# Kernel optimization log

Measured on AMD Instinct MI355X. Metric: run time of the kernel, lower is better.

Reference implementation:

```python
import jax, jax.numpy as jnp
import numpy as np

J = 24
ROOT = 0
# SMPL kinematic tree parents
PARENTS = [-1, 0, 0, 0, 1, 2, 3, 4, 5, 6, 7, 8, 9, 9, 9, 12, 13, 14, 16, 17, 18, 19, 20, 21]
RES_SCALE = 0.1


def rodrigues(rvec):
    """Axis-angle (..., 3) -> rotation matrix (..., 3, 3)."""
    theta = jnp.linalg.norm(rvec, axis=-1, keepdims=True)          # (...,1)
    axis = rvec / jnp.maximum(theta, 1e-8)
    x, y, z = axis[..., 0], axis[..., 1], axis[..., 2]
    zero = jnp.zeros_like(x)
    K = jnp.stack([zero, -z, y, z, zero, -x, -y, x, zero], axis=-1)
    K = K.reshape(rvec.shape[:-1] + (3, 3))
    s = jnp.sin(theta)[..., None]
    c = jnp.cos(theta)[..., None]
    I = jnp.eye(3, dtype=rvec.dtype)
    return I + s * K + (1.0 - c) * (K @ K)


def _make_T(R, t):
    """(B,3,3),(B,3) -> (B,4,4) homogeneous transform."""
    B = R.shape[0]
    top = jnp.concatenate([R, t[..., None]], axis=-1)              # (B,3,4)
    bottom = jnp.broadcast_to(jnp.array([0., 0., 0., 1.], R.dtype), (B, 1, 4))
    return jnp.concatenate([top, bottom], axis=-2)


def calculate_kinematic(rest_pose, rvecs, root_locs):
    """rest_pose (J,3), rvecs (B,J,3), root_locs (B,3) -> kp (B,J,3), skts (B,J,4,4).
    Sequential tree-structured chain, unrolled over the 24 joints."""
    R = rodrigues(rvecs)                                           # (B,J,3,3)
    B = rvecs.shape[0]
    l2w = [None] * J
    l2w[ROOT] = _make_T(R[:, ROOT], root_locs)
    for j in range(1, J):
        p = PARENTS[j]
        t_local = jnp.broadcast_to(rest_pose[j] - rest_pose[p], (B, 3))
        l2w[j] = l2w[p] @ _make_T(R[:, j], t_local)
    l2w = jnp.stack(l2w, axis=1)                                   # (B,J,4,4)
    kp = l2w[..., :3, 3]                                           # (B,J,3)
    # skts = inverse(l2w) = [R^T, -R^T t]
    Rt = jnp.swapaxes(l2w[..., :3, :3], -1, -2)
    t_inv = -(Rt @ kp[..., None])                                  # (B,J,3,1)
    top = jnp.concatenate([Rt, t_inv], axis=-1)                    # (B,J,3,4)
    bottom = jnp.broadcast_to(jnp.array([0., 0., 0., 1.], l2w.dtype), (B, J, 1, 4))
    skts = jnp.concatenate([top, bottom], axis=-2)                 # (B,J,4,4)
    return kp, skts


def setup_inputs() -> dict:
    key = jax.random.key(0)
    ks = jax.random.split(key, 12)
    N, NU, E, W = 131072, 16384, 16, 128
    skip = N // NU
    din, dout = J * 3 + E, J * 3 + 3
    bones = jax.random.normal(ks[0], (N, J, 3), jnp.float32) * 0.2
    pelvis_buf = jax.random.normal(ks[1], (NU, 3), jnp.float32)
    kp_idxs = jnp.arange(N, dtype=jnp.int64) // skip
    rest_pose = jax.random.normal(ks[2], (J, 3), jnp.float32) * 0.3
    rest_pose = rest_pose.at[ROOT].set(0.0)
    # kp3d root must match pelvis buffer (original asserts allclose)
    kp3d = jnp.zeros((N, J, 3), jnp.float32).at[:, ROOT].set(pelvis_buf[kp_idxs])
    emb_table = jax.random.normal(ks[3], (NU, E), jnp.float32) * 0.02
    def lin(k, fan_in, fan_out):
        lim = 1.0 / np.sqrt(fan_in)
        k1, k2 = jax.random.split(k)
        return (jax.random.uniform(k1, (fan_in, fan_out), jnp.float32, -lim, lim),
                jax.random.uniform(k2, (fan_out,), jnp.float32, -lim, lim))
    W0, b0 = lin(ks[4], din, W)
    W1, b1 = lin(ks[5], W, W)
    W2, b2 = lin(ks[6], W, W)
    W3, b3 = lin(ks[7], W, dout)
    return dict(bones=bones, kp3d=kp3d, kp_idxs=kp_idxs, emb_table=emb_table,
                pelvis_buf=pelvis_buf, rest_pose=rest_pose,
                W0=W0, b0=b0, W1=W1, b1=b1, W2=W2, b2=b2, W3=W3, b3=b3,
                N_unique=NU)


def reference(bones, kp3d, kp_idxs, emb_table, pelvis_buf, rest_pose,
              W0, b0, W1, b1, W2, b2, W3, b3, N_unique):
    N = bones.shape[0]
    skip = N // N_unique
    rvecs = bones[::skip].reshape(N_unique, J * 3)                 # (Nu, 72)
    kp_u = kp_idxs[::skip]
    embs = emb_table[kp_u]                                         # (Nu, 16)
    pelvis = pelvis_buf[kp_u]                                      # (Nu, 3)
    x = jnp.concatenate([rvecs, embs], axis=-1)
    h = jax.nn.relu(x @ W0 + b0)
    h = jax.nn.relu(h @ W1 + b1)
    h = jax.nn.relu(h @ W2 + b2)
    residual = (h @ W3 + b3) * RES_SCALE                           # (Nu, 75)
    rvecs = (rvecs + residual[:, :J * 3]).reshape(N_unique, J, 3)
    pelvis = pelvis + residual[:, J * 3:]
    kp, skts = calculate_kinematic(rest_pose, rvecs, pelvis)
    # expand unique poses back to full batch ('i s ... -> (i s) ...')
    kp = jnp.repeat(kp, skip, axis=0)                              # (N,J,3)
    skts = jnp.repeat(skts, skip, axis=0)                          # (N,J,4,4)
    rvecs = jnp.repeat(rvecs, skip, axis=0)                        # (N,J,3)
    return kp, skts, rvecs
```

## Files before the change

kernel.cpp:

```cpp
#include <hip/hip_runtime.h>
#include <hip/hip_bf16.h>

typedef unsigned short u16;
using f32x4 = __attribute__((ext_vector_type(4))) float;
using s16x8 = __attribute__((ext_vector_type(8))) short;
using u32x4 = __attribute__((ext_vector_type(4))) unsigned int;

#define JNT 24
#define STRX 104
#define STRH 136

__device__ __forceinline__ u16 f2bf(float f) {
    unsigned int x; __builtin_memcpy(&x, &f, 4);
    unsigned int lsb = (x >> 16) & 1u;
    x += 0x7fffu + lsb;
    return (u16)(x >> 16);
}

__global__ void prep_weights(const float* __restrict__ W0, const float* __restrict__ W1,
                             const float* __restrict__ W2, const float* __restrict__ W3,
                             u16* __restrict__ wst) {
    int i = blockIdx.x * 256 + threadIdx.x;
    if (i < 12288) { int n = i / 96, k = i - n * 96; wst[i] = (k < 88) ? f2bf(W0[k * 128 + n]) : (u16)0; return; }
    i -= 12288;
    if (i < 16384) { int n = i >> 7, k = i & 127; wst[12288 + i] = f2bf(W1[k * 128 + n]); return; }
    i -= 16384;
    if (i < 16384) { int n = i >> 7, k = i & 127; wst[28672 + i] = f2bf(W2[k * 128 + n]); return; }
    i -= 16384;
    if (i < 10240) { int n = i >> 7, k = i & 127; wst[45056 + i] = (n < 75) ? f2bf(W3[k * 75 + n]) : (u16)0; }
}

template<int BASE, int CNT>
__device__ __forceinline__ void mlp_l3(const u16* __restrict__ H, const u16* __restrict__ W3t,
                                       const float* __restrict__ b3, float* __restrict__ res_s,
                                       int lr, int lk, int drow) {
    f32x4 acc[CNT];
#pragma unroll
    for (int t = 0; t < CNT; ++t) {
        int col = (BASE + t) * 16 + lr;
        float bv = (col < 75) ? b3[col] : 0.f;
        acc[t] = (f32x4){bv, bv, bv, bv};
    }
#pragma unroll
    for (int ks = 0; ks < 4; ++ks) {
        s16x8 a = *(const s16x8*)&H[lr * STRH + ks * 32 + lk];
#pragma unroll
        for (int t = 0; t < CNT; ++t) {
            s16x8 b = *(const s16x8*)&W3t[((BASE + t) * 16 + lr) * 128 + ks * 32 + lk];
            acc[t] = __builtin_amdgcn_mfma_f32_16x16x32_bf16(a, b, acc[t], 0, 0, 0);
        }
    }
#pragma unroll
    for (int t = 0; t < CNT; ++t) {
        int col = (BASE + t) * 16 + lr;
        if (col < 75) {
#pragma unroll
            for (int q = 0; q < 4; ++q)
                res_s[(drow + q) * 80 + col] = acc[t][q] * 0.1f;
        }
    }
}

__device__ const int KPARP[32] = {0,0,0,0,1,2,3,4,5,6,7,8,9,9,9,12,13,14,16,17,18,19,20,21,0,0,0,0,0,0,0,0};
__device__ const int KDEPP[32] = {0,1,1,1,2,2,2,3,3,3,4,4,4,4,4,5,5,5,6,6,7,7,8,8,99,99,99,99,99,99,99,99};

__global__ __launch_bounds__(256, 3)
void fused_kernel(const float* __restrict__ bones, const float* __restrict__ emb,
                  const float* __restrict__ pelvis, const float* __restrict__ rest,
                  const float* __restrict__ b0, const float* __restrict__ b1,
                  const float* __restrict__ b2, const float* __restrict__ b3,
                  const u16* __restrict__ wst, float* __restrict__ out,
                  int N, int bstride) {
    __shared__ __align__(16) unsigned char smem[22016];
    float* res_s = (float*)smem;
    u16* Xs = (u16*)(smem + 5120);
    u16* H1 = (u16*)(smem + 8448);
    u16* H2 = (u16*)(smem + 12800);
    float* so8 = (float*)(smem + 5120);

    const int tid = threadIdx.x;
    const int row0 = blockIdx.x * 16;

    for (int i = tid; i < 16 * 96; i += 256) {
        int r = i / 96, c = i - r * 96;
        int u = row0 + r;
        float v = 0.f;
        if (c < 72)      v = bones[(size_t)u * bstride + c];
        else if (c < 88) v = emb[(size_t)u * 16 + (c - 72)];
        Xs[r * STRX + c] = f2bf(v);
    }
    __syncthreads();

    const int lane = tid & 63;
    const int wave = tid >> 6;
    const int lr = lane & 15;
    const int lk = (lane >> 4) * 8;
    const int drow = (lane >> 4) * 4;
    const u16* W0t = wst;
    const u16* W1t = wst + 12288;
    const u16* W2t = wst + 28672;
    const u16* W3t = wst + 45056;

    {
        f32x4 acc[2];
#pragma unroll
        for (int t = 0; t < 2; ++t) { float bv = b0[(wave * 2 + t) * 16 + lr]; acc[t] = (f32x4){bv, bv, bv, bv}; }
#pragma unroll
        for (int ks = 0; ks < 3; ++ks) {
            s16x8 a = *(const s16x8*)&Xs[lr * STRX + ks * 32 + lk];
#pragma unroll
            for (int t = 0; t < 2; ++t) {
                s16x8 b = *(const s16x8*)&W0t[((wave * 2 + t) * 16 + lr) * 96 + ks * 32 + lk];
                acc[t] = __builtin_amdgcn_mfma_f32_16x16x32_bf16(a, b, acc[t], 0, 0, 0);
            }
        }
#pragma unroll
        for (int t = 0; t < 2; ++t)
#pragma unroll
            for (int q = 0; q < 4; ++q)
                H1[(drow + q) * STRH + (wave * 2 + t) * 16 + lr] = f2bf(fmaxf(acc[t][q], 0.f));
    }
    __syncthreads();
    {
        f32x4 acc[2];
#pragma unroll
        for (int t = 0; t < 2; ++t) { float bv = b1[(wave * 2 + t) * 16 + lr]; acc[t] = (f32x4){bv, bv, bv, bv}; }
#pragma unroll
        for (int ks = 0; ks < 4; ++ks) {
            s16x8 a = *(const s16x8*)&H1[lr * STRH + ks * 32 + lk];
#pragma unroll
            for (int t = 0; t < 2; ++t) {
                s16x8 b = *(const s16x8*)&W1t[((wave * 2 + t) * 16 + lr) * 128 + ks * 32 + lk];
                acc[t] = __builtin_amdgcn_mfma_f32_16x16x32_bf16(a, b, acc[t], 0, 0, 0);
            }
        }
#pragma unroll
        for (int t = 0; t < 2; ++t)
#pragma unroll
            for (int q = 0; q < 4; ++q)
                H2[(drow + q) * STRH + (wave * 2 + t) * 16 + lr] = f2bf(fmaxf(acc[t][q], 0.f));
    }
    __syncthreads();
    {
        f32x4 acc[2];
#pragma unroll
        for (int t = 0; t < 2; ++t) { float bv = b2[(wave * 2 + t) * 16 + lr]; acc[t] = (f32x4){bv, bv, bv, bv}; }
#pragma unroll
        for (int ks = 0; ks < 4; ++ks) {
            s16x8 a = *(const s16x8*)&H2[lr * STRH + ks * 32 + lk];
#pragma unroll
            for (int t = 0; t < 2; ++t) {
                s16x8 b = *(const s16x8*)&W2t[((wave * 2 + t) * 16 + lr) * 128 + ks * 32 + lk];
                acc[t] = __builtin_amdgcn_mfma_f32_16x16x32_bf16(a, b, acc[t], 0, 0, 0);
            }
        }
        __syncthreads();
#pragma unroll
        for (int t = 0; t < 2; ++t)
#pragma unroll
            for (int q = 0; q < 4; ++q)
                H1[(drow + q) * STRH + (wave * 2 + t) * 16 + lr] = f2bf(fmaxf(acc[t][q], 0.f));
    }
    __syncthreads();
    if      (wave == 0) mlp_l3<0, 2>(H1, W3t, b3, res_s, lr, lk, drow);
    else if (wave == 1) mlp_l3<2, 1>(H1, W3t, b3, res_s, lr, lk, drow);
    else if (wave == 2) mlp_l3<3, 1>(H1, W3t, b3, res_s, lr, lk, drow);
    else                mlp_l3<4, 1>(H1, W3t, b3, res_s, lr, lk, drow);
    __syncthreads();

    const int half = lane >> 5, j = lane & 31;
    const int par = KPARP[j], dep = KDEPP[j];
    const int plane = (lane & 32) | par;

    const u32x4* ls = (const u32x4*)so8;
    u32x4* o4 = (u32x4*)out;
    const size_t r1 = (size_t)N * 18;
    const size_t r2 = (size_t)N * 114;

    for (int pass = 0; pass < 2; ++pass) {
        const int sloc8 = wave * 2 + half;
        const int sl = pass * 8 + sloc8;
        const size_t u = (size_t)row0 + sl;

        float R[3][3] = {{1.f,0.f,0.f},{0.f,1.f,0.f},{0.f,0.f,1.f}};
        float T[3] = {0.f, 0.f, 0.f};
        float rv0 = 0.f, rv1 = 0.f, rv2 = 0.f;

        if (j < JNT) {
            const float* rs = &res_s[sl * 80];
            const float* bn = &bones[u * (size_t)bstride];
            rv0 = bn[j * 3 + 0] + rs[j * 3 + 0];
            rv1 = bn[j * 3 + 1] + rs[j * 3 + 1];
            rv2 = bn[j * 3 + 2] + rs[j * 3 + 2];
            float th = sqrtf(rv0 * rv0 + rv1 * rv1 + rv2 * rv2);
            float s = sinf(th), c = cosf(th);
            float inv = 1.f / fmaxf(th, 1e-8f);
            float ax = rv0 * inv, ay = rv1 * inv, az = rv2 * inv;
            float K[3][3] = {{0.f, -az, ay}, {az, 0.f, -ax}, {-ay, ax, 0.f}};
            float KK[3][3];
#pragma unroll
            for (int r = 0; r < 3; ++r)
#pragma unroll
                for (int cc = 0; cc < 3; ++cc)
                    KK[r][cc] = K[r][0] * K[0][cc] + K[r][1] * K[1][cc] + K[r][2] * K[2][cc];
            float omc = 1.f - c;
#pragma unroll
            for (int r = 0; r < 3; ++r)
#pragma unroll
                for (int cc = 0; cc < 3; ++cc)
                    R[r][cc] = ((r == cc) ? 1.f : 0.f) + s * K[r][cc] + omc * KK[r][cc];
            if (j == 0) {
#pragma unroll
                for (int cc = 0; cc < 3; ++cc) T[cc] = pelvis[u * 3 + cc] + rs[72 + cc];
            } else {
#pragma unroll
                for (int cc = 0; cc < 3; ++cc) T[cc] = rest[j * 3 + cc] - rest[par * 3 + cc];
            }
        }

        for (int lev = 1; lev <= 8; ++lev) {
            float p00 = __shfl(R[0][0], plane), p01 = __shfl(R[0][1], plane), p02 = __shfl(R[0][2], plane);
            float p10 = __shfl(R[1][0], plane), p11 = __shfl(R[1][1], plane), p12 = __shfl(R[1][2], plane);
            float p20 = __shfl(R[2][0], plane), p21 = __shfl(R[2][1], plane), p22 = __shfl(R[2][2], plane);
            float q0  = __shfl(T[0],   plane), q1  = __shfl(T[1],   plane), q2  = __shfl(T[2],   plane);
            if (dep == lev) {
                float n00 = p00 * R[0][0] + p01 * R[1][0] + p02 * R[2][0];
                float n01 = p00 * R[0][1] + p01 * R[1][1] + p02 * R[2][1];
                float n02 = p00 * R[0][2] + p01 * R[1][2] + p02 * R[2][2];
                float n10 = p10 * R[0][0] + p11 * R[1][0] + p12 * R[2][0];
                float n11 = p10 * R[0][1] + p11 * R[1][1] + p12 * R[2][1];
                float n12 = p10 * R[0][2] + p11 * R[1][2] + p12 * R[2][2];
                float n20 = p20 * R[0][0] + p21 * R[1][0] + p22 * R[2][0];
                float n21 = p20 * R[0][1] + p21 * R[1][1] + p22 * R[2][1];
                float n22 = p20 * R[0][2] + p21 * R[1][2] + p22 * R[2][2];
                float m0  = p00 * T[0] + p01 * T[1] + p02 * T[2] + q0;
                float m1  = p10 * T[0] + p11 * T[1] + p12 * T[2] + q1;
                float m2  = p20 * T[0] + p21 * T[1] + p22 * T[2] + q2;
                R[0][0] = n00; R[0][1] = n01; R[0][2] = n02;
                R[1][0] = n10; R[1][1] = n11; R[1][2] = n12;
                R[2][0] = n20; R[2][1] = n21; R[2][2] = n22;
                T[0] = m0; T[1] = m1; T[2] = m2;
            }
        }

        if (j < JNT) {
            float* kp = &so8[sloc8 * 528 + j * 3];
            kp[0] = T[0]; kp[1] = T[1]; kp[2] = T[2];
            f32x4* sk4 = (f32x4*)&so8[sloc8 * 528 + 72 + j * 16];
#pragma unroll
            for (int r = 0; r < 3; ++r) {
                float ti = -(R[0][r] * T[0] + R[1][r] * T[1] + R[2][r] * T[2]);
                sk4[r] = (f32x4){R[0][r], R[1][r], R[2][r], ti};
            }
            sk4[3] = (f32x4){0.f, 0.f, 0.f, 1.f};
            float* rv = &so8[sloc8 * 528 + 456 + j * 3];
            rv[0] = rv0; rv[1] = rv1; rv[2] = rv2;
        }
        __syncthreads();

        for (int it = 0; it < 4; ++it) {
            int idx = tid + it * 256;
            int s = idx >> 7, p = idx & 127;
            size_t uu = (size_t)row0 + pass * 8 + s;
            u32x4 v = ls[s * 132 + p];
            if (p < 18) {
                u32x4* d = o4 + (uu * 144 + p);
#pragma unroll
                for (int rep = 0; rep < 8; ++rep) d[rep * 18] = v;
            } else if (p < 114) {
                u32x4* d = o4 + (r1 + uu * 768 + (p - 18));
#pragma unroll
                for (int rep = 0; rep < 8; ++rep) d[rep * 96] = v;
            } else {
                u32x4* d = o4 + (r2 + uu * 144 + (p - 114));
#pragma unroll
                for (int rep = 0; rep < 8; ++rep) d[rep * 18] = v;
            }
        }
        if (tid < 32) {
            int s = tid >> 2, p = 128 + (tid & 3);
            size_t uu = (size_t)row0 + pass * 8 + s;
            u32x4 v = ls[s * 132 + p];
            u32x4* d = o4 + (r2 + uu * 144 + (p - 114));
#pragma unroll
            for (int rep = 0; rep < 8; ++rep) d[rep * 18] = v;
        }
        __syncthreads();
    }
}

extern "C" void kernel_launch(void* const* d_in, const int* in_sizes, int n_in,
                              void* d_out, int out_size, void* d_ws, size_t ws_size,
                              hipStream_t stream) {
    const float* bones  = (const float*)d_in[0];
    const float* emb    = (const float*)d_in[3];
    const float* pelvis = (const float*)d_in[4];
    const float* rest   = (const float*)d_in[5];
    const float* W0 = (const float*)d_in[6];
    const float* b0 = (const float*)d_in[7];
    const float* W1 = (const float*)d_in[8];
    const float* b1 = (const float*)d_in[9];
    const float* W2 = (const float*)d_in[10];
    const float* b2 = (const float*)d_in[11];
    const float* W3 = (const float*)d_in[12];
    const float* b3 = (const float*)d_in[13];

    const int N    = in_sizes[0] / 72;
    const int NU   = in_sizes[3] / 16;
    const int skip = N / NU;
    const int bstride = skip * 72;

    u16* wst = (u16*)d_ws;

    prep_weights<<<216, 256, 0, stream>>>(W0, W1, W2, W3, wst);
    fused_kernel<<<NU / 16, 256, 0, stream>>>(bones, emb, pelvis, rest,
                                              b0, b1, b2, b3, wst,
                                              (float*)d_out, N, bstride);
}
```

Baseline: 71.68 us.

## Split output replication into a separate streaming kernel via staged workspace

```diff
diff --git a/kernel.cpp b/kernel.cpp
--- a/kernel.cpp
+++ b/kernel.cpp
@@ -69,8 +69,8 @@
                   const float* __restrict__ pelvis, const float* __restrict__ rest,
                   const float* __restrict__ b0, const float* __restrict__ b1,
                   const float* __restrict__ b2, const float* __restrict__ b3,
-                  const u16* __restrict__ wst, float* __restrict__ out,
-                  int N, int bstride) {
+                  const u16* __restrict__ wst, u32x4* __restrict__ staged,
+                  int bstride) {
     __shared__ __align__(16) unsigned char smem[22016];
     float* res_s = (float*)smem;
     u16* Xs = (u16*)(smem + 5120);
@@ -173,9 +173,6 @@
     const int plane = (lane & 32) | par;
 
     const u32x4* ls = (const u32x4*)so8;
-    u32x4* o4 = (u32x4*)out;
-    const size_t r1 = (size_t)N * 18;
-    const size_t r2 = (size_t)N * 114;
 
     for (int pass = 0; pass < 2; ++pass) {
         const int sloc8 = wave * 2 + half;
@@ -258,34 +255,33 @@
         }
         __syncthreads();
 
-        for (int it = 0; it < 4; ++it) {
-            int idx = tid + it * 256;
-            int s = idx >> 7, p = idx & 127;
-            size_t uu = (size_t)row0 + pass * 8 + s;
-            u32x4 v = ls[s * 132 + p];
-            if (p < 18) {
-                u32x4* d = o4 + (uu * 144 + p);
-#pragma unroll
-                for (int rep = 0; rep < 8; ++rep) d[rep * 18] = v;
-            } else if (p < 114) {
-                u32x4* d = o4 + (r1 + uu * 768 + (p - 18));
-#pragma unroll
-                for (int rep = 0; rep < 8; ++rep) d[rep * 96] = v;
-            } else {
-                u32x4* d = o4 + (r2 + uu * 144 + (p - 114));
-#pragma unroll
-                for (int rep = 0; rep < 8; ++rep) d[rep * 18] = v;
-            }
-        }
-        if (tid < 32) {
-            int s = tid >> 2, p = 128 + (tid & 3);
-            size_t uu = (size_t)row0 + pass * 8 + s;
-            u32x4 v = ls[s * 132 + p];
-            u32x4* d = o4 + (r2 + uu * 144 + (p - 114));
-#pragma unroll
-            for (int rep = 0; rep < 8; ++rep) d[rep * 18] = v;
-        }
+        u32x4* dst = staged + ((size_t)row0 + pass * 8) * 132;
+        for (int i = tid; i < 1056; i += 256)
+            dst[i] = ls[i];
         __syncthreads();
+    }
+}
+
+__global__ __launch_bounds__(256)
+void replicate_kernel(const u32x4* __restrict__ staged, u32x4* __restrict__ o4, int N) {
+    const int idx = blockIdx.x * 256 + threadIdx.x;
+    const int u = idx / 132;
+    const int p = idx - u * 132;
+    const u32x4 v = staged[idx];
+    const size_t r1 = (size_t)N * 18;
+    const size_t r2 = (size_t)N * 114;
+    if (p < 18) {
+        u32x4* d = o4 + ((size_t)u * 144 + p);
+#pragma unroll
+        for (int rep = 0; rep < 8; ++rep) d[rep * 18] = v;
+    } else if (p < 114) {
+        u32x4* d = o4 + (r1 + (size_t)u * 768 + (p - 18));
+#pragma unroll
+        for (int rep = 0; rep < 8; ++rep) d[rep * 96] = v;
+    } else {
+        u32x4* d = o4 + (r2 + (size_t)u * 144 + (p - 114));
+#pragma unroll
+        for (int rep = 0; rep < 8; ++rep) d[rep * 18] = v;
     }
 }
 
@@ -310,10 +306,12 @@
     const int skip = N / NU;
     const int bstride = skip * 72;
 
-    u16* wst = (u16*)d_ws;
+    u32x4* staged = (u32x4*)d_ws;
+    u16* wst = (u16*)((char*)d_ws + (size_t)NU * 132 * 16);
 
     prep_weights<<<216, 256, 0, stream>>>(W0, W1, W2, W3, wst);
     fused_kernel<<<NU / 16, 256, 0, stream>>>(bones, emb, pelvis, rest,
                                               b0, b1, b2, b3, wst,
-                                              (float*)d_out, N, bstride);
-}
+                                              staged, bstride);
+    replicate_kernel<<<NU * 132 / 256, 256, 0, stream>>>(staged, (u32x4*)d_out, N);
+}
```

Result: slower. 96.23 us (+34.2%).
